# Kernel optimization log

Hardware: AMD Instinct MI355X
Metric: run time of the kernel (lower is better)

## Reference

```python
import jax, jax.numpy as jnp
import numpy as np

TOP_K = 2

def setup_inputs() -> dict:
    key = jax.random.key(0)
    k0, k1, k2, k3 = jax.random.split(key, 4)
    B, T, D, F, E = 2, 2048, 1024, 4096, 8
    x = jax.random.normal(k0, (B, T, D), dtype=jnp.float32)
    Wr = jax.random.normal(k1, (E, D), dtype=jnp.float32) * 0.02   # router weight [out=E, in=D]
    W1 = jax.random.normal(k2, (E, F, D), dtype=jnp.float32) * 0.02  # per-expert up-proj [out=F, in=D]
    W2 = jax.random.normal(k3, (E, D, F), dtype=jnp.float32) * 0.02  # per-expert down-proj [out=D, in=F]
    return {"x": x, "Wr": Wr, "W1": W1, "W2": W2}

def reference(x, Wr, W1, W2):
    B, T, D = x.shape
    E = Wr.shape[0]
    N = B * T
    xf = x.reshape(N, D)
    # Router in fp32 on the un-cast activations (as in the torch module).
    logits = xf @ Wr.T                                   # [N, E]
    probs = jax.nn.softmax(logits, axis=-1)
    topk_w, topk_idx = jax.lax.top_k(probs, TOP_K)       # [N, K]
    topk_w = topk_w / jnp.sum(topk_w, axis=-1, keepdims=True)
    # Combine weights scattered into a dense [N, E] dispatch/combine matrix
    # (top_k indices are distinct, so .set is exact).
    combine = jnp.zeros((N, E), dtype=jnp.float32)
    combine = combine.at[jnp.arange(N)[:, None], topk_idx].set(topk_w)
    # Expert FFN runs in bf16 (comm_dtype in the original all-to-all pipeline).
    xb = xf.astype(jnp.bfloat16)
    h = jax.nn.gelu(jnp.einsum('nd,efd->enf', xb, W1.astype(jnp.bfloat16)),
                    approximate=False)                   # [E, N, F]
    yo = jnp.einsum('enf,edf->end', h, W2.astype(jnp.bfloat16))  # [E, N, D]
    # Weighted combine: bf16 expert outputs * fp32 gate weights -> fp32 (torch promotion).
    out = jnp.einsum('end,ne->nd', yo.astype(jnp.float32), combine)
    return out.reshape(B, T, D)
```

## Files before the change

### kernel.cpp

```cpp
#include <hip/hip_runtime.h>
#include <hip/hip_bf16.h>

typedef __attribute__((ext_vector_type(8))) __bf16 bf16x8;
typedef __attribute__((ext_vector_type(4))) float floatx4;

constexpr int N_TOK = 4096;
constexpr int DDIM  = 1024;
constexpr int FDIM  = 4096;
constexpr int NEXP  = 8;
constexpr int NSLOT = 2 * N_TOK;
constexpr int BM_T  = 256;
constexpr int MAXT  = NSLOT / BM_T + NEXP - 1;
constexpr int KSPLIT = 2;

static __device__ __forceinline__ unsigned short f2bf(float f) {
    union { __hip_bfloat16 h; unsigned short u; } v;
    v.h = __float2bfloat16(f);
    return v.u;
}

static __device__ __forceinline__ void gl2lds16(const unsigned short* g, unsigned short* l) {
    __builtin_amdgcn_global_load_lds(
        (__attribute__((address_space(1))) void*)g,
        (__attribute__((address_space(3))) void*)l,
        16, 0, 0);
}

__global__ void castW_kernel(const float* __restrict__ W1, const float* __restrict__ W2,
                             unsigned short* __restrict__ w1b, unsigned short* __restrict__ w2b,
                             int* __restrict__ counts) {
    constexpr int HALF = NEXP * FDIM * DDIM / 4;
    int i = blockIdx.x * 256 + threadIdx.x;
    const float* s; unsigned short* d; int j;
    if (i < HALF) { s = W1; d = w1b; j = i; }
    else          { s = W2; d = w2b; j = i - HALF; }
    float4 v = *(const float4*)(s + (size_t)j * 4);
    ushort4 o;
    o.x = f2bf(v.x); o.y = f2bf(v.y); o.z = f2bf(v.z); o.w = f2bf(v.w);
    *(ushort4*)(d + (size_t)j * 4) = o;
    if (blockIdx.x == 0 && threadIdx.x < NEXP) counts[threadIdx.x] = 0;
}

__global__ void router_kernel(const float* __restrict__ x, const float* __restrict__ Wr,
                              unsigned short* __restrict__ xb,
                              int* __restrict__ te, float* __restrict__ tw,
                              int* __restrict__ counts) {
    __shared__ float wr[NEXP * DDIM];
    const int tid = threadIdx.x;
    for (int i = tid; i < NEXP * DDIM; i += 256) wr[i] = Wr[i];
    __syncthreads();
    const int wave = tid >> 6, lane = tid & 63;
    const int t = blockIdx.x * 4 + wave;

    float xr[16];
    const float* xp = x + (size_t)t * DDIM;
    #pragma unroll
    for (int i = 0; i < 16; i++) xr[i] = xp[lane + 64 * i];

    unsigned short* xbp = xb + (size_t)t * DDIM;
    #pragma unroll
    for (int i = 0; i < 16; i++) xbp[lane + 64 * i] = f2bf(xr[i]);

    float logit[NEXP];
    #pragma unroll
    for (int e = 0; e < NEXP; e++) {
        float s = 0.f;
        #pragma unroll
        for (int i = 0; i < 16; i++) s += xr[i] * wr[e * DDIM + lane + 64 * i];
        #pragma unroll
        for (int off = 32; off > 0; off >>= 1) s += __shfl_xor(s, off, 64);
        logit[e] = s;
    }
    if (lane == 0) {
        int i0 = 0; float l0 = logit[0];
        #pragma unroll
        for (int e = 1; e < NEXP; e++) if (logit[e] > l0) { l0 = logit[e]; i0 = e; }
        int i1 = -1; float l1 = -3.0e38f;
        #pragma unroll
        for (int e = 0; e < NEXP; e++) if (e != i0 && logit[e] > l1) { l1 = logit[e]; i1 = e; }
        float p1 = expf(l1 - l0);
        float w0 = 1.f / (1.f + p1);
        float w1 = p1 * w0;
        te[t * 2] = i0; te[t * 2 + 1] = i1;
        tw[t * 2] = w0; tw[t * 2 + 1] = w1;
        atomicAdd(&counts[i0], 1);
        atomicAdd(&counts[i1], 1);
    }
}

__global__ void scan_scatter_kernel(const int* __restrict__ counts,
                                    const int* __restrict__ te, const float* __restrict__ tw,
                                    int* __restrict__ offsets, int* __restrict__ tile_em,
                                    int* __restrict__ ntile,
                                    int* __restrict__ rowid, float* __restrict__ gate,
                                    int* __restrict__ tok2slot) {
    __shared__ int soff[NEXP];
    __shared__ int scur[NEXP];
    const int tid = threadIdx.x;
    if (tid == 0) {
        int acc = 0, nt = 0;
        for (int e = 0; e < NEXP; e++) {
            offsets[e] = acc; soff[e] = acc;
            for (int m0 = 0; m0 < counts[e]; m0 += BM_T)
                tile_em[nt++] = (e << 16) | (m0 >> 8);
            acc += counts[e];
        }
        offsets[NEXP] = acc;
        ntile[0] = nt;
        for (int i = nt; i < MAXT; i++) tile_em[i] = 0;
    }
    if (tid < NEXP) scur[tid] = 0;
    __syncthreads();
    for (int t = tid; t < N_TOK; t += 256) {
        #pragma unroll
        for (int k = 0; k < 2; k++) {
            int e = te[t * 2 + k];
            int pos = atomicAdd(&scur[e], 1);
            int slot = soff[e] + pos;
            rowid[slot] = t;
            gate[slot] = tw[t * 2 + k];
            tok2slot[t * 2 + k] = slot;
        }
    }
}

template <bool UP>
__global__ __launch_bounds__(512, 4)
void ffn_gemm(const unsigned short* __restrict__ A,
              const unsigned short* __restrict__ Wb,
              unsigned short* __restrict__ Hout,
              float* __restrict__ Y,
              const int* __restrict__ rowid,
              const float* __restrict__ gate,
              const int* __restrict__ offsets,
              const int* __restrict__ tile_em,
              const int* __restrict__ ntile) {
    constexpr int BM = 256, BN = 128, BK = 32;
    constexpr int NOUT = UP ? FDIM : DDIM;
    constexpr int KDIM = UP ? DDIM : FDIM;
    constexpr int NN   = NOUT / BN;
    constexpr int KLEN = UP ? DDIM : (FDIM / KSPLIT);
    constexpr int KT   = KLEN / BK;
    constexpr int MREP = 4, NREP = 4;
    constexpr int ASTRIDE = BM * BK;
    constexpr int BSTRIDE = BN * BK;

    const int nwg = NN * MAXT * (UP ? 1 : KSPLIT);
    const int orig = blockIdx.x;
    const int xcd = orig & 7, idx = orig >> 3;
    const int qq = nwg >> 3, rr8 = nwg & 7;
    const int id = (xcd < rr8 ? xcd * (qq + 1) : rr8 * (qq + 1) + (xcd - rr8) * qq) + idx;

    const int n0 = (id % NN) * BN;
    const int bt = (id / NN) % MAXT;
    const int ks = UP ? 0 : (id / (NN * MAXT));
    if (bt >= ntile[0]) return;
    const int em = tile_em[bt];
    const int e  = em >> 16;
    const int m0 = (em & 0xffff) << 8;
    const int seg = offsets[e];
    const int cnt = offsets[e + 1] - seg;
    const int kbase = ks * KLEN;

    __shared__ __align__(16) unsigned short As[2 * ASTRIDE];
    __shared__ __align__(16) unsigned short Bs[2 * BSTRIDE];

    const int tid  = threadIdx.x;
    const int lane = tid & 63;
    const int wave = tid >> 6;
    const int lrow = lane >> 2;
    const int chunk = lane & 3;
    const int scol = (chunk ^ (lrow & 3)) * 8;

    const unsigned short* ag[2];
    #pragma unroll
    for (int j = 0; j < 2; j++) {
        int arow = wave * 32 + j * 16 + lrow;
        int slot = seg + m0 + arow;
        if (slot >= NSLOT) slot = NSLOT - 1;
        if (UP) { int t = rowid[slot]; ag[j] = A + (size_t)t * DDIM + kbase + scol; }
        else    { ag[j] = A + (size_t)slot * FDIM + kbase + scol; }
    }
    const unsigned short* bg0 =
        Wb + ((size_t)e * NOUT + n0 + wave * 16 + lrow) * KDIM + kbase + scol;

    unsigned short* asl[2];
    #pragma unroll
    for (int j = 0; j < 2; j++)
        asl[j] = &As[(wave * 32 + j * 16) * BK] + lane * 8;
    unsigned short* bsl0 = &Bs[(wave * 16) * BK] + lane * 8;

    auto stage = [&](int b) {
        gl2lds16(ag[0], asl[0] + b * ASTRIDE); ag[0] += BK;
        gl2lds16(ag[1], asl[1] + b * ASTRIDE); ag[1] += BK;
        gl2lds16(bg0,   bsl0   + b * BSTRIDE); bg0   += BK;
    };

    const int frow = lane & 15;
    const int quad = lane >> 4;
    const int wm = (wave >> 1) * 64;
    const int wn = (wave & 1) * 64;
    const int cs = ((quad ^ (frow & 3)) * 8);

    floatx4 acc[MREP][NREP];
    #pragma unroll
    for (int i = 0; i < MREP; i++)
        #pragma unroll
        for (int j = 0; j < NREP; j++)
            acc[i][j] = (floatx4){0.f, 0.f, 0.f, 0.f};

    stage(0);
    __syncthreads();
    for (int kt = 0; kt < KT; kt++) {
        if (kt + 1 < KT) stage((kt + 1) & 1);
        const unsigned short* Ab = &As[(kt & 1) * ASTRIDE];
        const unsigned short* Bb = &Bs[(kt & 1) * BSTRIDE];
        bf16x8 av[MREP], bv[NREP];
        #pragma unroll
        for (int i = 0; i < MREP; i++)
            av[i] = *(const bf16x8*)&Ab[(wm + i * 16 + frow) * BK + cs];
        #pragma unroll
        for (int j = 0; j < NREP; j++)
            bv[j] = *(const bf16x8*)&Bb[(wn + j * 16 + frow) * BK + cs];
        #pragma unroll
        for (int i = 0; i < MREP; i++)
            #pragma unroll
            for (int j = 0; j < NREP; j++)
                acc[i][j] = __builtin_amdgcn_mfma_f32_16x16x32_bf16(av[i], bv[j], acc[i][j], 0, 0, 0);
        __syncthreads();
    }

    #pragma unroll
    for (int mt = 0; mt < MREP; mt++) {
        #pragma unroll
        for (int rg = 0; rg < 4; rg++) {
            int mloc = m0 + wm + mt * 16 + quad * 4 + rg;
            if (mloc >= cnt) continue;
            int slot = seg + mloc;
            if (UP) {
                #pragma unroll
                for (int nt = 0; nt < NREP; nt++) {
                    int n = n0 + wn + nt * 16 + frow;
                    float v = acc[mt][nt][rg];
                    float g = 0.5f * v * (1.0f + erff(v * 0.70710678118654752f));
                    Hout[(size_t)slot * FDIM + n] = f2bf(g);
                }
            } else {
                float gw = gate[slot];
                #pragma unroll
                for (int nt = 0; nt < NREP; nt++) {
                    int n = n0 + wn + nt * 16 + frow;
                    Y[((size_t)ks * NSLOT + slot) * DDIM + n] = gw * acc[mt][nt][rg];
                }
            }
        }
    }
}

__global__ void combine_kernel(const float* __restrict__ Y, const int* __restrict__ tok2slot,
                               float* __restrict__ out) {
    int idx = blockIdx.x * 256 + threadIdx.x;
    int t = idx >> 8;
    int c = (idx & 255) * 4;
    int s0 = tok2slot[t * 2], s1 = tok2slot[t * 2 + 1];
    float4 r = make_float4(0.f, 0.f, 0.f, 0.f);
    #pragma unroll
    for (int ks = 0; ks < KSPLIT; ks++) {
        float4 a = *(const float4*)(Y + ((size_t)ks * NSLOT + s0) * DDIM + c);
        float4 b = *(const float4*)(Y + ((size_t)ks * NSLOT + s1) * DDIM + c);
        r.x += a.x + b.x; r.y += a.y + b.y; r.z += a.z + b.z; r.w += a.w + b.w;
    }
    *(float4*)(out + (size_t)t * DDIM + c) = r;
}

extern "C" void kernel_launch(void* const* d_in, const int* in_sizes, int n_in,
                              void* d_out, int out_size, void* d_ws, size_t ws_size,
                              hipStream_t stream) {
    const float* x  = (const float*)d_in[0];
    const float* Wr = (const float*)d_in[1];
    const float* W1 = (const float*)d_in[2];
    const float* W2 = (const float*)d_in[3];
    float* out = (float*)d_out;

    char* ws = (char*)d_ws;
    size_t off = 0;
    auto alloc = [&](size_t bytes) -> char* {
        char* p = ws + off;
        off = (off + bytes + 255) & ~(size_t)255;
        return p;
    };
    unsigned short* xb   = (unsigned short*)alloc((size_t)N_TOK * DDIM * 2);
    unsigned short* H    = (unsigned short*)alloc((size_t)NSLOT * FDIM * 2);
    float* Yb      = (float*)alloc((size_t)KSPLIT * NSLOT * DDIM * 4);
    int*   rowid   = (int*)alloc(NSLOT * 4);
    float* gatew   = (float*)alloc(NSLOT * 4);
    int*   te      = (int*)alloc(NSLOT * 4);
    float* tw      = (float*)alloc(NSLOT * 4);
    int*   t2s     = (int*)alloc(NSLOT * 4);
    int*   counts  = (int*)alloc(64);
    int*   offsets = (int*)alloc(64);
    int*   tile_em = (int*)alloc(MAXT * 4);
    int*   ntile   = (int*)alloc(64);
    unsigned short* w1b = (unsigned short*)alloc((size_t)NEXP * FDIM * DDIM * 2);
    unsigned short* w2b = (unsigned short*)alloc((size_t)NEXP * DDIM * FDIM * 2);
    (void)ws_size;

    constexpr int GRID_UP = (FDIM / 128) * MAXT;
    constexpr int GRID_DN = (DDIM / 128) * MAXT * KSPLIT;

    castW_kernel<<<2 * NEXP * FDIM * DDIM / 4 / 256, 256, 0, stream>>>(W1, W2, w1b, w2b, counts);
    router_kernel<<<N_TOK / 4, 256, 0, stream>>>(x, Wr, xb, te, tw, counts);
    scan_scatter_kernel<<<1, 256, 0, stream>>>(counts, te, tw, offsets, tile_em, ntile,
                                               rowid, gatew, t2s);
    ffn_gemm<true ><<<GRID_UP, 512, 0, stream>>>(xb, w1b, H, Yb, rowid, gatew,
                                                 offsets, tile_em, ntile);
    ffn_gemm<false><<<GRID_DN, 512, 0, stream>>>(H, w2b, H, Yb, rowid, gatew,
                                                 offsets, tile_em, ntile);
    combine_kernel<<<N_TOK, 256, 0, stream>>>(Yb, t2s, out);
}
```

Baseline: 683.9 us.

## Enlarge GEMM tiles to 256x256x64 with phased prefetch and merge prep kernels

The grouped expert GEMMs move from 256x128x32 tiles to 256x256x64 tiles with 8 waves per block. Each k-step is split into four phases that interleave async global-to-LDS loads with MFMA work, using explicit waitcnt, barriers and setprio. The down-projection uses a 4-way K split when the workspace is large enough, so more workgroups run at once. The weight-cast and router kernels are merged into one launch, and the counts reset becomes a memset. Larger tiles raise register pressure (launch bounds drop to 2 blocks per CU), and the 4-way split adds partial-sum traffic to the combine step.

New measurement: 809.9 us. 1.18x slower.

```diff
diff --git a/kernel.cpp b/kernel.cpp
--- a/kernel.cpp
+++ b/kernel.cpp
@@ -11,7 +11,6 @@
 constexpr int NSLOT = 2 * N_TOK;
 constexpr int BM_T  = 256;
 constexpr int MAXT  = NSLOT / BM_T + NEXP - 1;
-constexpr int KSPLIT = 2;
 
 static __device__ __forceinline__ unsigned short f2bf(float f) {
     union { __hip_bfloat16 h; unsigned short u; } v;
@@ -26,27 +25,27 @@
         16, 0, 0);
 }
 
-__global__ void castW_kernel(const float* __restrict__ W1, const float* __restrict__ W2,
-                             unsigned short* __restrict__ w1b, unsigned short* __restrict__ w2b,
-                             int* __restrict__ counts) {
-    constexpr int HALF = NEXP * FDIM * DDIM / 4;
-    int i = blockIdx.x * 256 + threadIdx.x;
-    const float* s; unsigned short* d; int j;
-    if (i < HALF) { s = W1; d = w1b; j = i; }
-    else          { s = W2; d = w2b; j = i - HALF; }
-    float4 v = *(const float4*)(s + (size_t)j * 4);
-    ushort4 o;
-    o.x = f2bf(v.x); o.y = f2bf(v.y); o.z = f2bf(v.z); o.w = f2bf(v.w);
-    *(ushort4*)(d + (size_t)j * 4) = o;
-    if (blockIdx.x == 0 && threadIdx.x < NEXP) counts[threadIdx.x] = 0;
-}
-
-__global__ void router_kernel(const float* __restrict__ x, const float* __restrict__ Wr,
-                              unsigned short* __restrict__ xb,
-                              int* __restrict__ te, float* __restrict__ tw,
-                              int* __restrict__ counts) {
+__global__ void prep_kernel(const float* __restrict__ x, const float* __restrict__ Wr,
+                            const float* __restrict__ W1, const float* __restrict__ W2,
+                            unsigned short* __restrict__ xb,
+                            unsigned short* __restrict__ w1b, unsigned short* __restrict__ w2b,
+                            int* __restrict__ te, float* __restrict__ tw,
+                            int* __restrict__ counts) {
+    constexpr int RBLK = N_TOK / 4;
     __shared__ float wr[NEXP * DDIM];
     const int tid = threadIdx.x;
+    if (blockIdx.x >= RBLK) {
+        constexpr int HALF = NEXP * FDIM * DDIM / 4;
+        int i = (blockIdx.x - RBLK) * 256 + tid;
+        const float* s; unsigned short* d; int j;
+        if (i < HALF) { s = W1; d = w1b; j = i; }
+        else          { s = W2; d = w2b; j = i - HALF; }
+        float4 v = *(const float4*)(s + (size_t)j * 4);
+        ushort4 o;
+        o.x = f2bf(v.x); o.y = f2bf(v.y); o.z = f2bf(v.z); o.w = f2bf(v.w);
+        *(ushort4*)(d + (size_t)j * 4) = o;
+        return;
+    }
     for (int i = tid; i < NEXP * DDIM; i += 256) wr[i] = Wr[i];
     __syncthreads();
     const int wave = tid >> 6, lane = tid & 63;
@@ -124,8 +123,8 @@
     }
 }
 
-template <bool UP>
-__global__ __launch_bounds__(512, 4)
+template <bool UP, int KS>
+__global__ __launch_bounds__(512, 2)
 void ffn_gemm(const unsigned short* __restrict__ A,
               const unsigned short* __restrict__ Wb,
               unsigned short* __restrict__ Hout,
@@ -135,17 +134,15 @@
               const int* __restrict__ offsets,
               const int* __restrict__ tile_em,
               const int* __restrict__ ntile) {
-    constexpr int BM = 256, BN = 128, BK = 32;
+    constexpr int BM = 256, BN = 256, BK = 64;
     constexpr int NOUT = UP ? FDIM : DDIM;
     constexpr int KDIM = UP ? DDIM : FDIM;
     constexpr int NN   = NOUT / BN;
-    constexpr int KLEN = UP ? DDIM : (FDIM / KSPLIT);
+    constexpr int KLEN = UP ? DDIM : (FDIM / KS);
     constexpr int KT   = KLEN / BK;
-    constexpr int MREP = 4, NREP = 4;
-    constexpr int ASTRIDE = BM * BK;
-    constexpr int BSTRIDE = BN * BK;
-
-    const int nwg = NN * MAXT * (UP ? 1 : KSPLIT);
+    constexpr int AST  = BM * BK;
+
+    const int nwg = NN * MAXT * (UP ? 1 : KS);
     const int orig = blockIdx.x;
     const int xcd = orig & 7, idx = orig >> 3;
     const int qq = nwg >> 3, rr8 = nwg & 7;
@@ -162,76 +159,117 @@
     const int cnt = offsets[e + 1] - seg;
     const int kbase = ks * KLEN;
 
-    __shared__ __align__(16) unsigned short As[2 * ASTRIDE];
-    __shared__ __align__(16) unsigned short Bs[2 * BSTRIDE];
+    __shared__ __align__(16) unsigned short As[2 * AST];
+    __shared__ __align__(16) unsigned short Bs[2 * AST];
 
     const int tid  = threadIdx.x;
     const int lane = tid & 63;
     const int wave = tid >> 6;
-    const int lrow = lane >> 2;
-    const int chunk = lane & 3;
-    const int scol = (chunk ^ (lrow & 3)) * 8;
-
-    const unsigned short* ag[2];
-    #pragma unroll
-    for (int j = 0; j < 2; j++) {
-        int arow = wave * 32 + j * 16 + lrow;
-        int slot = seg + m0 + arow;
-        if (slot >= NSLOT) slot = NSLOT - 1;
-        if (UP) { int t = rowid[slot]; ag[j] = A + (size_t)t * DDIM + kbase + scol; }
-        else    { ag[j] = A + (size_t)slot * FDIM + kbase + scol; }
-    }
-    const unsigned short* bg0 =
-        Wb + ((size_t)e * NOUT + n0 + wave * 16 + lrow) * KDIM + kbase + scol;
-
-    unsigned short* asl[2];
-    #pragma unroll
-    for (int j = 0; j < 2; j++)
-        asl[j] = &As[(wave * 32 + j * 16) * BK] + lane * 8;
-    unsigned short* bsl0 = &Bs[(wave * 16) * BK] + lane * 8;
-
-    auto stage = [&](int b) {
-        gl2lds16(ag[0], asl[0] + b * ASTRIDE); ag[0] += BK;
-        gl2lds16(ag[1], asl[1] + b * ASTRIDE); ag[1] += BK;
-        gl2lds16(bg0,   bsl0   + b * BSTRIDE); bg0   += BK;
+    const int lrow = lane >> 3;
+    const int chunk = lane & 7;
+    const int scoff = (chunk ^ lrow) * 8;
+    const int h = wave >> 2;
+
+    const unsigned short* gA[2][2]; int dA[2][2];
+    #pragma unroll
+    for (int pp = 0; pp < 2; pp++) {
+        #pragma unroll
+        for (int j = 0; j < 2; j++) {
+            int o = pp * 8 + (wave & 3) * 2 + j;
+            int rl = h * 128 + o * 8 + lrow;
+            dA[pp][j] = (h * 128 + o * 8) * BK + lane * 8;
+            int slot = seg + m0 + rl;
+            if (slot >= NSLOT) slot = NSLOT - 1;
+            if (UP) { int trow = rowid[slot]; gA[pp][j] = A + (size_t)trow * KDIM + kbase + scoff; }
+            else    { gA[pp][j] = A + (size_t)slot * KDIM + kbase + scoff; }
+        }
+    }
+    const unsigned short* gB[2][2]; int dB[2][2];
+    #pragma unroll
+    for (int pp = 0; pp < 2; pp++) {
+        #pragma unroll
+        for (int j = 0; j < 2; j++) {
+            int o = ((wave >> 1) & 1) * 8 + pp * 4 + (wave & 1) * 2 + j;
+            int rl = h * 128 + o * 8 + lrow;
+            dB[pp][j] = (h * 128 + o * 8) * BK + lane * 8;
+            gB[pp][j] = Wb + ((size_t)e * NOUT + n0 + rl) * KDIM + kbase + scoff;
+        }
+    }
+
+    auto stA = [&](int pp, int b) {
+        gl2lds16(gA[pp][0], &As[b * AST + dA[pp][0]]); gA[pp][0] += BK;
+        gl2lds16(gA[pp][1], &As[b * AST + dA[pp][1]]); gA[pp][1] += BK;
+    };
+    auto stB = [&](int pp, int b) {
+        gl2lds16(gB[pp][0], &Bs[b * AST + dB[pp][0]]); gB[pp][0] += BK;
+        gl2lds16(gB[pp][1], &Bs[b * AST + dB[pp][1]]); gB[pp][1] += BK;
     };
 
     const int frow = lane & 15;
     const int quad = lane >> 4;
-    const int wm = (wave >> 1) * 64;
-    const int wn = (wave & 1) * 64;
-    const int cs = ((quad ^ (frow & 3)) * 8);
-
-    floatx4 acc[MREP][NREP];
-    #pragma unroll
-    for (int i = 0; i < MREP; i++)
-        #pragma unroll
-        for (int j = 0; j < NREP; j++)
+    const int fx   = frow & 7;
+    const int wm = (wave >> 2) * 128;
+    const int wn = (wave & 3) * 64;
+
+    floatx4 acc[8][4];
+    #pragma unroll
+    for (int i = 0; i < 8; i++)
+        #pragma unroll
+        for (int j = 0; j < 4; j++)
             acc[i][j] = (floatx4){0.f, 0.f, 0.f, 0.f};
 
-    stage(0);
-    __syncthreads();
-    for (int kt = 0; kt < KT; kt++) {
-        if (kt + 1 < KT) stage((kt + 1) & 1);
-        const unsigned short* Ab = &As[(kt & 1) * ASTRIDE];
-        const unsigned short* Bb = &Bs[(kt & 1) * BSTRIDE];
-        bf16x8 av[MREP], bv[NREP];
-        #pragma unroll
-        for (int i = 0; i < MREP; i++)
-            av[i] = *(const bf16x8*)&Ab[(wm + i * 16 + frow) * BK + cs];
-        #pragma unroll
-        for (int j = 0; j < NREP; j++)
-            bv[j] = *(const bf16x8*)&Bb[(wn + j * 16 + frow) * BK + cs];
-        #pragma unroll
-        for (int i = 0; i < MREP; i++)
+    stA(0, 0); stB(0, 0); stB(1, 0); stA(1, 0);
+    asm volatile("s_waitcnt vmcnt(0)" ::: "memory");
+    __builtin_amdgcn_s_barrier();
+
+    for (int t = 0; t < KT; ++t) {
+        const int pb = t & 1;
+        const bool more = (t + 1 < KT);
+        #pragma unroll
+        for (int ph = 0; ph < 4; ++ph) {
+            if (more) {
+                if      (ph == 0) stA(0, pb ^ 1);
+                else if (ph == 1) stB(0, pb ^ 1);
+                else if (ph == 2) stB(1, pb ^ 1);
+                else              stA(1, pb ^ 1);
+            }
+            const int mh = ph >> 1, nh = ph & 1;
+            bf16x8 av[4][2], bv[2][2];
             #pragma unroll
-            for (int j = 0; j < NREP; j++)
-                acc[i][j] = __builtin_amdgcn_mfma_f32_16x16x32_bf16(av[i], bv[j], acc[i][j], 0, 0, 0);
-        __syncthreads();
-    }
-
-    #pragma unroll
-    for (int mt = 0; mt < MREP; mt++) {
+            for (int i = 0; i < 4; i++)
+                #pragma unroll
+                for (int kk = 0; kk < 2; kk++)
+                    av[i][kk] = *(const bf16x8*)&As[pb * AST + (wm + mh * 64 + i * 16 + frow) * BK
+                                                   + (((kk * 4 + quad) ^ fx) * 8)];
+            #pragma unroll
+            for (int j = 0; j < 2; j++)
+                #pragma unroll
+                for (int kk = 0; kk < 2; kk++)
+                    bv[j][kk] = *(const bf16x8*)&Bs[pb * AST + (wn + nh * 32 + j * 16 + frow) * BK
+                                                   + (((kk * 4 + quad) ^ fx) * 8)];
+            if (more)        asm volatile("s_waitcnt vmcnt(4) lgkmcnt(0)" ::: "memory");
+            else if (ph == 0) asm volatile("s_waitcnt vmcnt(2) lgkmcnt(0)" ::: "memory");
+            else              asm volatile("s_waitcnt vmcnt(0) lgkmcnt(0)" ::: "memory");
+            __builtin_amdgcn_s_barrier();
+            __builtin_amdgcn_sched_barrier(0);
+            __builtin_amdgcn_s_setprio(1);
+            #pragma unroll
+            for (int i = 0; i < 4; i++)
+                #pragma unroll
+                for (int j = 0; j < 2; j++) {
+                    acc[mh * 4 + i][nh * 2 + j] =
+                        __builtin_amdgcn_mfma_f32_16x16x32_bf16(av[i][0], bv[j][0],
+                                                                acc[mh * 4 + i][nh * 2 + j], 0, 0, 0);
+                    acc[mh * 4 + i][nh * 2 + j] =
+                        __builtin_amdgcn_mfma_f32_16x16x32_bf16(av[i][1], bv[j][1],
+                                                                acc[mh * 4 + i][nh * 2 + j], 0, 0, 0);
+                }
+            __builtin_amdgcn_s_setprio(0);
+        }
+    }
+
+    #pragma unroll
+    for (int mt = 0; mt < 8; mt++) {
         #pragma unroll
         for (int rg = 0; rg < 4; rg++) {
             int mloc = m0 + wm + mt * 16 + quad * 4 + rg;
@@ -239,7 +277,7 @@
             int slot = seg + mloc;
             if (UP) {
                 #pragma unroll
-                for (int nt = 0; nt < NREP; nt++) {
+                for (int nt = 0; nt < 4; nt++) {
                     int n = n0 + wn + nt * 16 + frow;
                     float v = acc[mt][nt][rg];
                     float g = 0.5f * v * (1.0f + erff(v * 0.70710678118654752f));
@@ -248,7 +286,7 @@
             } else {
                 float gw = gate[slot];
                 #pragma unroll
-                for (int nt = 0; nt < NREP; nt++) {
+                for (int nt = 0; nt < 4; nt++) {
                     int n = n0 + wn + nt * 16 + frow;
                     Y[((size_t)ks * NSLOT + slot) * DDIM + n] = gw * acc[mt][nt][rg];
                 }
@@ -258,14 +296,13 @@
 }
 
 __global__ void combine_kernel(const float* __restrict__ Y, const int* __restrict__ tok2slot,
-                               float* __restrict__ out) {
+                               float* __restrict__ out, int nks) {
     int idx = blockIdx.x * 256 + threadIdx.x;
     int t = idx >> 8;
     int c = (idx & 255) * 4;
     int s0 = tok2slot[t * 2], s1 = tok2slot[t * 2 + 1];
     float4 r = make_float4(0.f, 0.f, 0.f, 0.f);
-    #pragma unroll
-    for (int ks = 0; ks < KSPLIT; ks++) {
+    for (int ks = 0; ks < nks; ks++) {
         float4 a = *(const float4*)(Y + ((size_t)ks * NSLOT + s0) * DDIM + c);
         float4 b = *(const float4*)(Y + ((size_t)ks * NSLOT + s1) * DDIM + c);
         r.x += a.x + b.x; r.y += a.y + b.y; r.z += a.z + b.z; r.w += a.w + b.w;
@@ -281,6 +318,22 @@
     const float* W1 = (const float*)d_in[2];
     const float* W2 = (const float*)d_in[3];
     float* out = (float*)d_out;
+
+    auto plan = [&](int nks, size_t& total) {
+        size_t off = 0;
+        auto sz = [&](size_t bytes) { size_t p = off; off = (off + bytes + 255) & ~(size_t)255; return p; };
+        sz((size_t)N_TOK * DDIM * 2);
+        sz((size_t)NSLOT * FDIM * 2);
+        sz((size_t)nks * NSLOT * DDIM * 4);
+        sz(NSLOT * 4); sz(NSLOT * 4); sz(NSLOT * 4); sz(NSLOT * 4); sz(NSLOT * 4);
+        sz(64); sz(64); sz(MAXT * 4); sz(64);
+        sz((size_t)NEXP * FDIM * DDIM * 2);
+        sz((size_t)NEXP * DDIM * FDIM * 2);
+        total = off;
+    };
+    size_t need4, need2;
+    plan(4, need4); plan(2, need2);
+    const int nks = (need4 <= ws_size) ? 4 : 2;
 
     char* ws = (char*)d_ws;
     size_t off = 0;
@@ -291,7 +344,7 @@
     };
     unsigned short* xb   = (unsigned short*)alloc((size_t)N_TOK * DDIM * 2);
     unsigned short* H    = (unsigned short*)alloc((size_t)NSLOT * FDIM * 2);
-    float* Yb      = (float*)alloc((size_t)KSPLIT * NSLOT * DDIM * 4);
+    float* Yb      = (float*)alloc((size_t)nks * NSLOT * DDIM * 4);
     int*   rowid   = (int*)alloc(NSLOT * 4);
     float* gatew   = (float*)alloc(NSLOT * 4);
     int*   te      = (int*)alloc(NSLOT * 4);
@@ -305,16 +358,22 @@
     unsigned short* w2b = (unsigned short*)alloc((size_t)NEXP * DDIM * FDIM * 2);
     (void)ws_size;
 
-    constexpr int GRID_UP = (FDIM / 128) * MAXT;
-    constexpr int GRID_DN = (DDIM / 128) * MAXT * KSPLIT;
-
-    castW_kernel<<<2 * NEXP * FDIM * DDIM / 4 / 256, 256, 0, stream>>>(W1, W2, w1b, w2b, counts);
-    router_kernel<<<N_TOK / 4, 256, 0, stream>>>(x, Wr, xb, te, tw, counts);
+    constexpr int RBLK = N_TOK / 4;
+    constexpr int CBLK = 2 * NEXP * FDIM * DDIM / 4 / 256;
+    constexpr int GRID_UP = (FDIM / 256) * MAXT;
+
+    hipMemsetAsync(counts, 0, NEXP * sizeof(int), stream);
+    prep_kernel<<<RBLK + CBLK, 256, 0, stream>>>(x, Wr, W1, W2, xb, w1b, w2b, te, tw, counts);
     scan_scatter_kernel<<<1, 256, 0, stream>>>(counts, te, tw, offsets, tile_em, ntile,
                                                rowid, gatew, t2s);
-    ffn_gemm<true ><<<GRID_UP, 512, 0, stream>>>(xb, w1b, H, Yb, rowid, gatew,
-                                                 offsets, tile_em, ntile);
-    ffn_gemm<false><<<GRID_DN, 512, 0, stream>>>(H, w2b, H, Yb, rowid, gatew,
-                                                 offsets, tile_em, ntile);
-    combine_kernel<<<N_TOK, 256, 0, stream>>>(Yb, t2s, out);
-}
+    ffn_gemm<true, 1><<<GRID_UP, 512, 0, stream>>>(xb, w1b, H, Yb, rowid, gatew,
+                                                   offsets, tile_em, ntile);
+    if (nks == 4) {
+        ffn_gemm<false, 4><<<(DDIM / 256) * MAXT * 4, 512, 0, stream>>>(H, w2b, H, Yb, rowid, gatew,
+                                                                        offsets, tile_em, ntile);
+    } else {
+        ffn_gemm<false, 2><<<(DDIM / 256) * MAXT * 2, 512, 0, stream>>>(H, w2b, H, Yb, rowid, gatew,
+                                                                        offsets, tile_em, ntile);
+    }
+    combine_kernel<<<N_TOK, 256, 0, stream>>>(Yb, t2s, out, nks);
+}
```
